# Optimization experiments

Hardware: AMD Instinct MI355X
Metric: run time of the kernel (lower is better)

## Reference

```python
import jax, jax.numpy as jnp
import numpy as np

B, Nq, C, H = 1, 300, 256, 8
h, w = 32, 32
HW = h * w
HID = 512  # rpe_hidden_dim
HD = C // H


def setup_inputs() -> dict:
    key = jax.random.key(0)
    ks = jax.random.split(key, 16)
    s = 0.02
    inp = {
        "raw_query": jax.random.normal(ks[0], (B, Nq, C), jnp.float32),
        "query_pos": jax.random.normal(ks[1], (B, Nq, C), jnp.float32),
        "reference_points": jax.random.uniform(ks[2], (B, Nq, 2), jnp.float32),
        "raw_src": jax.random.normal(ks[3], (B, HW, C), jnp.float32),
        "src_pos_embed": jax.random.normal(ks[4], (B, HW, C), jnp.float32),
        "Wq": jax.random.normal(ks[5], (C, C), jnp.float32) * s,
        "bq": jnp.zeros((C,), jnp.float32),
        "Wk": jax.random.normal(ks[6], (C, C), jnp.float32) * s,
        "bk": jnp.zeros((C,), jnp.float32),
        "Wv": jax.random.normal(ks[7], (C, C), jnp.float32) * s,
        "bv": jnp.zeros((C,), jnp.float32),
        "Wo": jax.random.normal(ks[8], (C, C), jnp.float32) * s,
        "bo": jnp.zeros((C,), jnp.float32),
        "W1": jax.random.normal(ks[9], (HID, 2), jnp.float32),   # cpb MLP layer 1
        "b1": jnp.zeros((HID,), jnp.float32),
        "W2": jax.random.normal(ks[10], (H, HID), jnp.float32) * s,  # cpb MLP layer 2 (no bias)
        "input_spatial_shapes": np.array([[h, w]], dtype=np.int64),
    }
    return inp


def _key_positions(hh, ww):
    ys = (jnp.arange(hh, dtype=jnp.float32) + 0.5) / hh
    xs = (jnp.arange(ww, dtype=jnp.float32) + 0.5) / ww
    yy, xx = jnp.meshgrid(ys, xs, indexing="ij")  # row-major: idx = y*w + x
    return jnp.stack([xx.ravel(), yy.ravel()], axis=-1)  # [HW, 2] (x, y)


def reference(raw_query, query_pos, reference_points, raw_src, src_pos_embed,
              Wq, bq, Wk, bk, Wv, bv, Wo, bo, W1, b1, W2, input_spatial_shapes):
    hh, ww = int(input_spatial_shapes[0, 0]), int(input_spatial_shapes[0, 1])
    scale = HD ** (-0.5)
    queries = raw_query + query_pos                      # [B,Nq,C]
    memory = raw_src + src_pos_embed                     # [B,HW,C]

    q = (queries @ Wq.T + bq).reshape(B, Nq, H, HD)
    k = (memory @ Wk.T + bk).reshape(B, hh * ww, H, HD)
    v = (memory @ Wv.T + bv).reshape(B, hh * ww, H, HD)

    logits = jnp.einsum("bqhd,bkhd->bhqk", q, k) * scale  # [B,H,Nq,HW]

    key_pos = _key_positions(hh, ww)                      # [HW,2]
    delta = reference_points[:, :, None, :] - key_pos[None, None]  # [B,Nq,HW,2]
    hid = jax.nn.relu(jnp.einsum("bqkc,hc->bqkh", delta, W1) + b1)  # [B,Nq,HW,HID]
    bias = jnp.einsum("bqkf,hf->bhqk", hid, W2)           # [B,H,Nq,HW]

    attn = jax.nn.softmax(logits + bias, axis=-1)
    out = jnp.einsum("bhqk,bkhd->bqhd", attn, v).reshape(B, Nq, C)
    return out @ Wo.T + bo
```

## Files before the change

kernel.cpp:

```cpp
#include <hip/hip_runtime.h>
#include <hip/hip_fp16.h>
#include <stdint.h>

#define NQ   300
#define CDIM 256
#define NH   8
#define HD   32
#define HWK  1024
#define HIDD 512

typedef __attribute__((ext_vector_type(8))) _Float16 f16x8;
typedef __attribute__((ext_vector_type(2))) _Float16 h2v;
typedef __attribute__((ext_vector_type(4))) float f32x4;

#define QB_OFF   0
#define KB_OFF   153600
#define VT_OFF   677888
#define PO_OFF   1202176
#define PL_OFF   3659776
#define A16_OFF  3736576
#define NX_OFF   4043776
#define NY_OFF   4044800
#define W2_OFF   4045824

__device__ __forceinline__ short f16b(float x){
  _Float16 h = (_Float16)x;
  return __builtin_bit_cast(short, h);
}

__device__ __forceinline__ uint32_t pk_f16(float a, float b){
  auto r = __builtin_amdgcn_cvt_pkrtz(a, b);
  return __builtin_bit_cast(uint32_t, r);
}

__device__ __forceinline__ h2v cvt2h(float a, float b){
  auto r = __builtin_amdgcn_cvt_pkrtz(a, b);
  return __builtin_bit_cast(h2v, r);
}

__global__ __launch_bounds__(256) void prep_kernel(
    const float* __restrict__ refp, const float* __restrict__ W1,
    const float* __restrict__ b1, const float* __restrict__ W2,
    short* __restrict__ a16, short* __restrict__ nx16,
    short* __restrict__ ny16, short* __restrict__ w216)
{
  int idx = blockIdx.x * 256 + threadIdx.x;
  if (idx < NQ*HIDD){
    int q = idx >> 9, f = idx & 511;
    float2 w = ((const float2*)W1)[f];
    float a = fmaf(w.x, refp[2*q], fmaf(w.y, refp[2*q+1], b1[f]));
    a16[idx] = f16b(a);
  } else {
    int j = idx - NQ*HIDD;
    if (j < HIDD){
      float2 w = ((const float2*)W1)[j];
      nx16[j] = f16b(-w.x);
      ny16[j] = f16b(-w.y);
    } else if (j < HIDD + NH*HIDD){
      int e = j - HIDD;
      w216[e] = f16b(W2[e]);
    }
  }
}

__global__ __launch_bounds__(256) void proj_kernel(
    const float* __restrict__ rq, const float* __restrict__ qp,
    const float* __restrict__ rs, const float* __restrict__ spe,
    const float* __restrict__ Wq, const float* __restrict__ bq,
    const float* __restrict__ Wk, const float* __restrict__ bk,
    const float* __restrict__ Wv, const float* __restrict__ bv,
    const float* __restrict__ Wo, const float* __restrict__ bo,
    char* __restrict__ ws, float* __restrict__ dout, int final_mode)
{
  int bxid = blockIdx.x;
  int tile = bxid >> 1, half = bxid & 1;
  const float *in1, *in2, *W, *bias;
  int r0, M, mode;
  const float* po = (const float*)(ws + PO_OFF);
  const float* pl = (const float*)(ws + PL_OFF);
  if (final_mode){
    in1 = po; in2 = nullptr; W = Wo; bias = bo;
    r0 = tile*16; M = NQ; mode = 3;
  } else if (tile < 19){
    in1 = rq; in2 = qp; W = Wq; bias = bq; r0 = tile*16; M = NQ; mode = 0;
  } else if (tile < 83){
    in1 = rs; in2 = spe; W = Wk; bias = bk; r0 = (tile-19)*16; M = HWK; mode = 1;
  } else {
    in1 = rs; in2 = spe; W = Wv; bias = bv; r0 = (tile-83)*16; M = HWK; mode = 2;
  }
  __shared__ __align__(16) float At[32][20];
  __shared__ float Wl[32][129];
  __shared__ float linv[16][8];
  int tid = threadIdx.x;
  int n_loc = tid & 127;
  int rg = tid >> 7;
  int n = half*128 + n_loc;
  float acc[8];
  float bv_ = bias[n];
  #pragma unroll
  for (int i=0;i<8;i++) acc[i] = bv_;

  if (mode == 3 && tid < 128){
    int r = tid >> 3, hh = tid & 7;
    int gr = r0 + r; if (gr >= M) gr = M - 1;
    float s = 0.f;
    #pragma unroll
    for (int p = 0; p < 8; p++) s += pl[((size_t)p*NQ+gr)*NH+hh];
    linv[r][hh] = 1.0f / s;
  }

  for (int c0 = 0; c0 < CDIM; c0 += 32){
    __syncthreads();
    for (int e = tid; e < 512; e += 256){
      int r = e >> 5, c = e & 31;
      int gr = r0 + r; if (gr >= M) gr = M - 1;
      float v;
      if (mode == 3){
        int cc = c0 + c;
        v = 0.f;
        #pragma unroll
        for (int p = 0; p < 8; p++) v += po[(size_t)(p*NQ+gr)*CDIM + cc];
        v *= linv[r][c0 >> 5];
      } else {
        v = in1[gr*CDIM + c0 + c];
        if (in2) v += in2[gr*CDIM + c0 + c];
      }
      At[c][r] = v;
    }
    for (int e = tid; e < 4096; e += 256){
      int c = e & 31, nn = e >> 5;
      Wl[c][nn] = W[(half*128 + nn)*CDIM + c0 + c];
    }
    __syncthreads();
    #pragma unroll
    for (int c = 0; c < 32; c++){
      float w = Wl[c][n_loc];
      const float4* ap = (const float4*)&At[c][rg*8];
      float4 a0 = ap[0], a1 = ap[1];
      acc[0] = fmaf(a0.x, w, acc[0]);
      acc[1] = fmaf(a0.y, w, acc[1]);
      acc[2] = fmaf(a0.z, w, acc[2]);
      acc[3] = fmaf(a0.w, w, acc[3]);
      acc[4] = fmaf(a1.x, w, acc[4]);
      acc[5] = fmaf(a1.y, w, acc[5]);
      acc[6] = fmaf(a1.z, w, acc[6]);
      acc[7] = fmaf(a1.w, w, acc[7]);
    }
  }

  if (mode == 0){
    short* qb = (short*)(ws + QB_OFF);
    const float s = 0.17677669529663687f;
    #pragma unroll
    for (int i=0;i<8;i++){
      int gr = r0 + rg*8 + i;
      if (gr < M) qb[gr*CDIM + n] = f16b(acc[i]*s);
    }
  } else if (mode == 1){
    short* kb = (short*)(ws + KB_OFF);
    int h = n >> 5, d = n & 31;
    #pragma unroll
    for (int i=0;i<8;i++){
      int gr = r0 + rg*8 + i;
      if (gr < M) kb[((size_t)h*HWK + gr)*HD + d] = f16b(acc[i]);
    }
  } else if (mode == 2){
    short* vt = (short*)(ws + VT_OFF);
    uint32_t p[4];
    #pragma unroll
    for (int i=0;i<4;i++) p[i] = pk_f16(acc[2*i], acc[2*i+1]);
    *(uint4*)(vt + n*HWK + r0 + rg*8) = make_uint4(p[0], p[1], p[2], p[3]);
  } else {
    #pragma unroll
    for (int i=0;i<8;i++){
      int gr = r0 + rg*8 + i;
      if (gr < M) dout[gr*CDIM + n] = acc[i];
    }
  }
}

__global__ __launch_bounds__(256, 4) void fused_kernel(
    const short* __restrict__ a16, const short* __restrict__ nx16,
    const short* __restrict__ ny16, const short* __restrict__ w216,
    const short* __restrict__ qb, const short* __restrict__ kb,
    const short* __restrict__ vt, float* __restrict__ po,
    float* __restrict__ pl)
{
  int bid = blockIdx.x;
  int q0 = (bid >> 3) * 2, kr = bid & 7;
  int tid = threadIdx.x, wave = tid >> 6, lane = tid & 63;
  int n = lane & 15, qd = lane >> 4;

  __shared__ __align__(16) _Float16 nwx[HIDD];
  __shared__ __align__(16) char pool[8192];
  __shared__ __align__(16) _Float16 w2l[NH][520];
  __shared__ __align__(16) _Float16 pb[2][NH][136];
  __shared__ float lsum[4][16];
  _Float16 (*c1s)[4][HIDD] = (_Float16 (*)[4][HIDD])pool;
  float (*part)[4][NH][32] = (float (*)[4][NH][32])pool;

  {
    int f0 = tid * 2;
    h2v ny2 = *(const h2v*)(ny16 + f0);
    h2v nx2 = *(const h2v*)(nx16 + f0);
    *(h2v*)&nwx[f0] = nx2;
    #pragma unroll
    for (int qq = 0; qq < 2; qq++){
      h2v a2 = *(const h2v*)(a16 + (q0+qq)*HIDD + f0);
      #pragma unroll
      for (int r = 0; r < 4; r++){
        _Float16 kyh = (_Float16)(((float)(kr*4 + r) + 0.5f) * (1.0f/32.0f));
        h2v ky2 = {kyh, kyh};
        *(h2v*)&c1s[qq][r][f0] = ny2 * ky2 + a2;
      }
    }
  }
  for (int e = tid; e < 512; e += 256){
    int r = e >> 6, c = e & 63;
    *(f16x8*)&w2l[r][c*8] = *(const f16x8*)(w216 + r*HIDD + c*8);
  }
  f16x8 qfrag = *(const f16x8*)(qb + (q0 + (n >> 3))*CDIM + (n & 7)*HD + qd*8);
  f16x8 qm[NH];
  #pragma unroll
  for (int h = 0; h < NH; h++){
    f16x8 z = {0,0,0,0,0,0,0,0};
    qm[h] = ((n & 7) == h) ? qfrag : z;
  }
  __syncthreads();

  const int kyrow = kr*4 + wave;
  const int kbase = kyrow * 32;

  f32x4 acc1[2] = {{0.f,0.f,0.f,0.f},{0.f,0.f,0.f,0.f}};
  #pragma unroll
  for (int t = 0; t < 2; t++){
    int k0 = kbase + t*16;
    #pragma unroll
    for (int h = 0; h < NH; h++){
      f16x8 af = *(const f16x8*)(kb + ((size_t)h*HWK + k0 + n)*HD + qd*8);
      acc1[t] = __builtin_amdgcn_mfma_f32_16x16x32_f16(af, qm[h], acc1[t], 0, 0, 0);
    }
  }

  _Float16 kxAh = (_Float16)(((float)n + 0.5f) * (1.0f/32.0f));
  _Float16 kxBh = (_Float16)(((float)n + 16.5f) * (1.0f/32.0f));
  f16x8 kxA8, kxB8, z8;
  #pragma unroll
  for (int j = 0; j < 8; j++){ kxA8[j] = kxAh; kxB8[j] = kxBh; z8[j] = (_Float16)0.f; }
  f32x4 accb[2][2];
  accb[0][0] = acc1[0]; accb[0][1] = acc1[1];
  accb[1][0] = acc1[0]; accb[1][1] = acc1[1];
  const _Float16* c1r0 = &c1s[0][wave][0];
  const _Float16* c1r1 = &c1s[1][wave][0];
  #pragma unroll 4
  for (int kc = 0; kc < 16; kc++){
    int f0 = kc*32 + qd*8;
    f16x8 c10 = *(const f16x8*)(c1r0 + f0);
    f16x8 c11 = *(const f16x8*)(c1r1 + f0);
    f16x8 wxv = *(const f16x8*)(&nwx[f0]);
    f16x8 bfr = *(const f16x8*)(&w2l[n & 7][f0]);
    #pragma unroll
    for (int t = 0; t < 2; t++){
      f16x8 kx8 = t ? kxB8 : kxA8;
      f16x8 e0 = __builtin_elementwise_max(wxv * kx8 + c10, z8);
      accb[0][t] = __builtin_amdgcn_mfma_f32_16x16x32_f16(e0, bfr, accb[0][t], 0, 0, 0);
      f16x8 e1 = __builtin_elementwise_max(wxv * kx8 + c11, z8);
      accb[1][t] = __builtin_amdgcn_mfma_f32_16x16x32_f16(e1, bfr, accb[1][t], 0, 0, 0);
    }
  }

  int qsel = n >> 3, hsel = n & 7;
  float lacc = 0.f;
  #pragma unroll
  for (int t = 0; t < 2; t++){
    f32x4 a = qsel ? accb[1][t] : accb[0][t];
    float e0 = __expf(a[0]);
    float e1 = __expf(a[1]);
    float e2 = __expf(a[2]);
    float e3 = __expf(a[3]);
    uint2 p2;
    p2.x = pk_f16(e0, e1);
    p2.y = pk_f16(e2, e3);
    *(uint2*)&pb[qsel][hsel][wave*32 + t*16 + qd*4] = p2;
    float s = e0 + e1 + e2 + e3;
    s += __shfl_xor(s, 16);
    s += __shfl_xor(s, 32);
    lacc += s;
  }
  if (lane < 16) lsum[wave][lane] = lacc;

  #pragma unroll
  for (int h = 0; h < NH; h++){
    int kl = wave*32 + qd*8;
    f16x8 pa = *(const f16x8*)&pb[n & 1][h][kl];
    f16x8 v0 = *(const f16x8*)(vt + ((size_t)(h*HD +      n))*HWK + kr*128 + kl);
    f16x8 v1 = *(const f16x8*)(vt + ((size_t)(h*HD + 16 + n))*HWK + kr*128 + kl);
    f32x4 o0 = {0.f,0.f,0.f,0.f}, o1 = {0.f,0.f,0.f,0.f};
    o0 = __builtin_amdgcn_mfma_f32_16x16x32_f16(pa, v0, o0, 0, 0, 0);
    o1 = __builtin_amdgcn_mfma_f32_16x16x32_f16(pa, v1, o1, 0, 0, 0);
    if (qd == 0){
      part[0][wave][h][n]      = o0[0];
      part[1][wave][h][n]      = o0[1];
      part[0][wave][h][16 + n] = o1[0];
      part[1][wave][h][16 + n] = o1[1];
    }
  }
  __syncthreads();

  {
    int h = tid >> 5, d = tid & 31;
    #pragma unroll
    for (int qq = 0; qq < 2; qq++){
      float s = part[qq][0][h][d] + part[qq][1][h][d]
              + part[qq][2][h][d] + part[qq][3][h][d];
      po[((size_t)kr*NQ + q0 + qq)*CDIM + tid] = s;
    }
    if (tid < 16){
      float s = lsum[0][tid] + lsum[1][tid] + lsum[2][tid] + lsum[3][tid];
      pl[((size_t)kr*NQ + q0 + (tid >> 3))*NH + (tid & 7)] = s;
    }
  }
}

extern "C" void kernel_launch(void* const* d_in, const int* in_sizes, int n_in,
                              void* d_out, int out_size, void* d_ws, size_t ws_size,
                              hipStream_t stream)
{
  const float* rq  = (const float*)d_in[0];
  const float* qp  = (const float*)d_in[1];
  const float* rp  = (const float*)d_in[2];
  const float* rs  = (const float*)d_in[3];
  const float* spe = (const float*)d_in[4];
  const float* Wq  = (const float*)d_in[5];
  const float* bq  = (const float*)d_in[6];
  const float* Wk  = (const float*)d_in[7];
  const float* bk  = (const float*)d_in[8];
  const float* Wv  = (const float*)d_in[9];
  const float* bv  = (const float*)d_in[10];
  const float* Wo  = (const float*)d_in[11];
  const float* bo  = (const float*)d_in[12];
  const float* W1  = (const float*)d_in[13];
  const float* b1  = (const float*)d_in[14];
  const float* W2  = (const float*)d_in[15];
  char* ws = (char*)d_ws;
  float* dout = (float*)d_out;

  prep_kernel<<<618, 256, 0, stream>>>(rp, W1, b1, W2,
      (short*)(ws + A16_OFF), (short*)(ws + NX_OFF),
      (short*)(ws + NY_OFF), (short*)(ws + W2_OFF));
  proj_kernel<<<294, 256, 0, stream>>>(rq, qp, rs, spe, Wq, bq, Wk, bk,
      Wv, bv, Wo, bo, ws, dout, 0);
  fused_kernel<<<1200, 256, 0, stream>>>((const short*)(ws + A16_OFF),
      (const short*)(ws + NX_OFF), (const short*)(ws + NY_OFF),
      (const short*)(ws + W2_OFF), (const short*)(ws + QB_OFF),
      (const short*)(ws + KB_OFF), (const short*)(ws + VT_OFF),
      (float*)(ws + PO_OFF), (float*)(ws + PL_OFF));
  proj_kernel<<<38, 256, 0, stream>>>(rq, qp, rs, spe, Wq, bq, Wk, bk,
      Wv, bv, Wo, bo, ws, dout, 1);
}
```

Baseline: 154.5 us.

## Merge prep into projection kernel and split QKV tiles into quarters

The separate prep kernel is folded into the projection launch as extra trailing blocks, which removes one kernel launch. The QKV projection now splits each row tile into four 64-column quarters instead of two 128-column halves, doubling the block count to improve occupancy and shrinking per-thread accumulators. The final output projection moves into its own specialized kernel with no mode branching. In exchange, each block reloads the input tile more often across the extra column splits.

```diff
diff --git a/kernel.cpp b/kernel.cpp
--- a/kernel.cpp
+++ b/kernel.cpp
@@ -33,55 +33,42 @@
   return __builtin_bit_cast(uint32_t, r);
 }
 
-__device__ __forceinline__ h2v cvt2h(float a, float b){
-  auto r = __builtin_amdgcn_cvt_pkrtz(a, b);
-  return __builtin_bit_cast(h2v, r);
-}
-
-__global__ __launch_bounds__(256) void prep_kernel(
-    const float* __restrict__ refp, const float* __restrict__ W1,
-    const float* __restrict__ b1, const float* __restrict__ W2,
-    short* __restrict__ a16, short* __restrict__ nx16,
-    short* __restrict__ ny16, short* __restrict__ w216)
-{
-  int idx = blockIdx.x * 256 + threadIdx.x;
-  if (idx < NQ*HIDD){
-    int q = idx >> 9, f = idx & 511;
-    float2 w = ((const float2*)W1)[f];
-    float a = fmaf(w.x, refp[2*q], fmaf(w.y, refp[2*q+1], b1[f]));
-    a16[idx] = f16b(a);
-  } else {
-    int j = idx - NQ*HIDD;
-    if (j < HIDD){
-      float2 w = ((const float2*)W1)[j];
-      nx16[j] = f16b(-w.x);
-      ny16[j] = f16b(-w.y);
-    } else if (j < HIDD + NH*HIDD){
-      int e = j - HIDD;
-      w216[e] = f16b(W2[e]);
-    }
-  }
-}
-
 __global__ __launch_bounds__(256) void proj_kernel(
     const float* __restrict__ rq, const float* __restrict__ qp,
     const float* __restrict__ rs, const float* __restrict__ spe,
     const float* __restrict__ Wq, const float* __restrict__ bq,
     const float* __restrict__ Wk, const float* __restrict__ bk,
     const float* __restrict__ Wv, const float* __restrict__ bv,
-    const float* __restrict__ Wo, const float* __restrict__ bo,
-    char* __restrict__ ws, float* __restrict__ dout, int final_mode)
+    const float* __restrict__ refp, const float* __restrict__ W1,
+    const float* __restrict__ b1, const float* __restrict__ W2,
+    char* __restrict__ ws)
 {
   int bxid = blockIdx.x;
-  int tile = bxid >> 1, half = bxid & 1;
+  int tid = threadIdx.x;
+
+  if (bxid >= 588){
+    int pidx = (bxid - 588)*256 + tid;
+    if (pidx < 153600){
+      int q = pidx >> 9, f = pidx & 511;
+      float2 w = ((const float2*)W1)[f];
+      float a = fmaf(w.x, refp[2*q], fmaf(w.y, refp[2*q+1], b1[f]));
+      ((short*)(ws + A16_OFF))[pidx] = f16b(a);
+    } else if (pidx < 154112){
+      int f = pidx - 153600;
+      float2 w = ((const float2*)W1)[f];
+      ((short*)(ws + NX_OFF))[f] = f16b(-w.x);
+      ((short*)(ws + NY_OFF))[f] = f16b(-w.y);
+    } else if (pidx < 158208){
+      int e = pidx - 154112;
+      ((short*)(ws + W2_OFF))[e] = f16b(W2[e]);
+    }
+    return;
+  }
+
+  int tile = bxid >> 2, quarter = bxid & 3;
   const float *in1, *in2, *W, *bias;
   int r0, M, mode;
-  const float* po = (const float*)(ws + PO_OFF);
-  const float* pl = (const float*)(ws + PL_OFF);
-  if (final_mode){
-    in1 = po; in2 = nullptr; W = Wo; bias = bo;
-    r0 = tile*16; M = NQ; mode = 3;
-  } else if (tile < 19){
+  if (tile < 19){
     in1 = rq; in2 = qp; W = Wq; bias = bq; r0 = tile*16; M = NQ; mode = 0;
   } else if (tile < 83){
     in1 = rs; in2 = spe; W = Wk; bias = bk; r0 = (tile-19)*16; M = HWK; mode = 1;
@@ -89,62 +76,37 @@
     in1 = rs; in2 = spe; W = Wv; bias = bv; r0 = (tile-83)*16; M = HWK; mode = 2;
   }
   __shared__ __align__(16) float At[32][20];
-  __shared__ float Wl[32][129];
-  __shared__ float linv[16][8];
-  int tid = threadIdx.x;
-  int n_loc = tid & 127;
-  int rg = tid >> 7;
-  int n = half*128 + n_loc;
-  float acc[8];
+  __shared__ float Wl[32][68];
+  int nq = tid & 63;
+  int rg = tid >> 6;
+  int n = quarter*64 + nq;
+  float acc[4];
   float bv_ = bias[n];
   #pragma unroll
-  for (int i=0;i<8;i++) acc[i] = bv_;
-
-  if (mode == 3 && tid < 128){
-    int r = tid >> 3, hh = tid & 7;
-    int gr = r0 + r; if (gr >= M) gr = M - 1;
-    float s = 0.f;
-    #pragma unroll
-    for (int p = 0; p < 8; p++) s += pl[((size_t)p*NQ+gr)*NH+hh];
-    linv[r][hh] = 1.0f / s;
-  }
+  for (int i=0;i<4;i++) acc[i] = bv_;
 
   for (int c0 = 0; c0 < CDIM; c0 += 32){
     __syncthreads();
     for (int e = tid; e < 512; e += 256){
       int r = e >> 5, c = e & 31;
       int gr = r0 + r; if (gr >= M) gr = M - 1;
-      float v;
-      if (mode == 3){
-        int cc = c0 + c;
-        v = 0.f;
-        #pragma unroll
-        for (int p = 0; p < 8; p++) v += po[(size_t)(p*NQ+gr)*CDIM + cc];
-        v *= linv[r][c0 >> 5];
-      } else {
-        v = in1[gr*CDIM + c0 + c];
-        if (in2) v += in2[gr*CDIM + c0 + c];
-      }
+      float v = in1[gr*CDIM + c0 + c];
+      if (in2) v += in2[gr*CDIM + c0 + c];
       At[c][r] = v;
     }
-    for (int e = tid; e < 4096; e += 256){
+    for (int e = tid; e < 2048; e += 256){
       int c = e & 31, nn = e >> 5;
-      Wl[c][nn] = W[(half*128 + nn)*CDIM + c0 + c];
+      Wl[c][nn] = W[(quarter*64 + nn)*CDIM + c0 + c];
     }
     __syncthreads();
     #pragma unroll
     for (int c = 0; c < 32; c++){
-      float w = Wl[c][n_loc];
-      const float4* ap = (const float4*)&At[c][rg*8];
-      float4 a0 = ap[0], a1 = ap[1];
-      acc[0] = fmaf(a0.x, w, acc[0]);
-      acc[1] = fmaf(a0.y, w, acc[1]);
-      acc[2] = fmaf(a0.z, w, acc[2]);
-      acc[3] = fmaf(a0.w, w, acc[3]);
-      acc[4] = fmaf(a1.x, w, acc[4]);
-      acc[5] = fmaf(a1.y, w, acc[5]);
-      acc[6] = fmaf(a1.z, w, acc[6]);
-      acc[7] = fmaf(a1.w, w, acc[7]);
+      float w = Wl[c][nq];
+      float4 a = *(const float4*)&At[c][rg*4];
+      acc[0] = fmaf(a.x, w, acc[0]);
+      acc[1] = fmaf(a.y, w, acc[1]);
+      acc[2] = fmaf(a.z, w, acc[2]);
+      acc[3] = fmaf(a.w, w, acc[3]);
     }
   }
 
@@ -152,30 +114,24 @@
     short* qb = (short*)(ws + QB_OFF);
     const float s = 0.17677669529663687f;
     #pragma unroll
-    for (int i=0;i<8;i++){
-      int gr = r0 + rg*8 + i;
+    for (int i=0;i<4;i++){
+      int gr = r0 + rg*4 + i;
       if (gr < M) qb[gr*CDIM + n] = f16b(acc[i]*s);
     }
   } else if (mode == 1){
     short* kb = (short*)(ws + KB_OFF);
     int h = n >> 5, d = n & 31;
     #pragma unroll
-    for (int i=0;i<8;i++){
-      int gr = r0 + rg*8 + i;
+    for (int i=0;i<4;i++){
+      int gr = r0 + rg*4 + i;
       if (gr < M) kb[((size_t)h*HWK + gr)*HD + d] = f16b(acc[i]);
     }
-  } else if (mode == 2){
+  } else {
     short* vt = (short*)(ws + VT_OFF);
-    uint32_t p[4];
-    #pragma unroll
-    for (int i=0;i<4;i++) p[i] = pk_f16(acc[2*i], acc[2*i+1]);
-    *(uint4*)(vt + n*HWK + r0 + rg*8) = make_uint4(p[0], p[1], p[2], p[3]);
-  } else {
-    #pragma unroll
-    for (int i=0;i<8;i++){
-      int gr = r0 + rg*8 + i;
-      if (gr < M) dout[gr*CDIM + n] = acc[i];
-    }
+    uint2 p2;
+    p2.x = pk_f16(acc[0], acc[1]);
+    p2.y = pk_f16(acc[2], acc[3]);
+    *(uint2*)(vt + n*HWK + r0 + rg*4) = p2;
   }
 }
 
@@ -319,6 +275,74 @@
       float s = lsum[0][tid] + lsum[1][tid] + lsum[2][tid] + lsum[3][tid];
       pl[((size_t)kr*NQ + q0 + (tid >> 3))*NH + (tid & 7)] = s;
     }
+  }
+}
+
+__global__ __launch_bounds__(256) void projf_kernel(
+    const float* __restrict__ Wo, const float* __restrict__ bo,
+    char* __restrict__ ws, float* __restrict__ dout)
+{
+  int bxid = blockIdx.x;
+  int tile = bxid >> 1, half = bxid & 1;
+  const float* po = (const float*)(ws + PO_OFF);
+  const float* pl = (const float*)(ws + PL_OFF);
+  int r0 = tile*16, M = NQ;
+  __shared__ __align__(16) float At[32][20];
+  __shared__ float Wl[32][129];
+  __shared__ float linv[16][8];
+  int tid = threadIdx.x;
+  int n_loc = tid & 127;
+  int rg = tid >> 7;
+  int n = half*128 + n_loc;
+  float acc[8];
+  float bv_ = bo[n];
+  #pragma unroll
+  for (int i=0;i<8;i++) acc[i] = bv_;
+
+  if (tid < 128){
+    int r = tid >> 3, hh = tid & 7;
+    int gr = r0 + r; if (gr >= M) gr = M - 1;
+    float s = 0.f;
+    #pragma unroll
+    for (int p = 0; p < 8; p++) s += pl[((size_t)p*NQ+gr)*NH+hh];
+    linv[r][hh] = 1.0f / s;
+  }
+
+  for (int c0 = 0; c0 < CDIM; c0 += 32){
+    __syncthreads();
+    for (int e = tid; e < 512; e += 256){
+      int r = e >> 5, c = e & 31;
+      int gr = r0 + r; if (gr >= M) gr = M - 1;
+      int cc = c0 + c;
+      float v = 0.f;
+      #pragma unroll
+      for (int p = 0; p < 8; p++) v += po[(size_t)(p*NQ+gr)*CDIM + cc];
+      At[c][r] = v * linv[r][c0 >> 5];
+    }
+    for (int e = tid; e < 4096; e += 256){
+      int c = e & 31, nn = e >> 5;
+      Wl[c][nn] = Wo[(half*128 + nn)*CDIM + c0 + c];
+    }
+    __syncthreads();
+    #pragma unroll
+    for (int c = 0; c < 32; c++){
+      float w = Wl[c][n_loc];
+      const float4* ap = (const float4*)&At[c][rg*8];
+      float4 a0 = ap[0], a1 = ap[1];
+      acc[0] = fmaf(a0.x, w, acc[0]);
+      acc[1] = fmaf(a0.y, w, acc[1]);
+      acc[2] = fmaf(a0.z, w, acc[2]);
+      acc[3] = fmaf(a0.w, w, acc[3]);
+      acc[4] = fmaf(a1.x, w, acc[4]);
+      acc[5] = fmaf(a1.y, w, acc[5]);
+      acc[6] = fmaf(a1.z, w, acc[6]);
+      acc[7] = fmaf(a1.w, w, acc[7]);
+    }
+  }
+  #pragma unroll
+  for (int i=0;i<8;i++){
+    int gr = r0 + rg*8 + i;
+    if (gr < M) dout[gr*CDIM + n] = acc[i];
   }
 }
 
@@ -345,16 +369,12 @@
   char* ws = (char*)d_ws;
   float* dout = (float*)d_out;
 
-  prep_kernel<<<618, 256, 0, stream>>>(rp, W1, b1, W2,
-      (short*)(ws + A16_OFF), (short*)(ws + NX_OFF),
-      (short*)(ws + NY_OFF), (short*)(ws + W2_OFF));
-  proj_kernel<<<294, 256, 0, stream>>>(rq, qp, rs, spe, Wq, bq, Wk, bk,
-      Wv, bv, Wo, bo, ws, dout, 0);
+  proj_kernel<<<1206, 256, 0, stream>>>(rq, qp, rs, spe, Wq, bq, Wk, bk,
+      Wv, bv, rp, W1, b1, W2, ws);
   fused_kernel<<<1200, 256, 0, stream>>>((const short*)(ws + A16_OFF),
       (const short*)(ws + NX_OFF), (const short*)(ws + NY_OFF),
       (const short*)(ws + W2_OFF), (const short*)(ws + QB_OFF),
       (const short*)(ws + KB_OFF), (const short*)(ws + VT_OFF),
       (float*)(ws + PO_OFF), (float*)(ws + PL_OFF));
-  proj_kernel<<<38, 256, 0, stream>>>(rq, qp, rs, spe, Wq, bq, Wk, bk,
-      Wv, bv, Wo, bo, ws, dout, 1);
-}
+  projf_kernel<<<38, 256, 0, stream>>>(Wo, bo, ws, dout);
+}
```

Result: no change. 155.0 us (+0.3%).
